# Performance work log

Hardware: AMD Instinct MI355X
Metric: run time of the kernel (lower is better)

## Reference

```python
import jax, jax.numpy as jnp
import numpy as np

H = 256          # hidden_channels
NP, NJ, NC = 8192, 8192, 4096  # person / job_posting / company node counts
EA, EW, EP = 262144, 131072, 131072  # edge counts per relation


def _gcn(x_src, W, b, edge_index, num_src, num_dst):
    """Bipartite GCNConv: h = x_src @ W; out[dst] = sum_e norm_e * h[src_e] + b,
    norm = deg_out(src)^-1/2 * deg_in(dst)^-1/2 (symmetric GCN normalization)."""
    h = x_src @ W                                # [num_src, H]
    row, col = edge_index[0], edge_index[1]
    ones = jnp.ones(row.shape[0], dtype=h.dtype)
    deg_src = jax.ops.segment_sum(ones, row, num_segments=num_src)
    deg_dst = jax.ops.segment_sum(ones, col, num_segments=num_dst)
    dis_src = jnp.where(deg_src > 0, jax.lax.rsqrt(jnp.maximum(deg_src, 1e-12)), 0.0)
    dis_dst = jnp.where(deg_dst > 0, jax.lax.rsqrt(jnp.maximum(deg_dst, 1e-12)), 0.0)
    norm = dis_src[row] * dis_dst[col]           # [E]
    out = jax.ops.segment_sum(h[row] * norm[:, None], col, num_segments=num_dst)
    return out + b


def setup_inputs() -> dict:
    key = jax.random.key(0)
    ks = jax.random.split(key, 12)
    s = 1.0 / np.sqrt(H)
    return {
        "x_person":  jax.random.normal(ks[0], (NP, H), jnp.float32),
        "x_job":     jax.random.normal(ks[1], (NJ, H), jnp.float32),
        "x_company": jax.random.normal(ks[2], (NC, H), jnp.float32),
        "ei_applied": jax.random.randint(ks[3], (2, EA), 0, 8192, jnp.int64 if jax.config.read('jax_enable_x64') else jnp.int32),
        "ei_worked":  jax.random.randint(ks[4], (2, EW), 0, 4096, jnp.int64 if jax.config.read('jax_enable_x64') else jnp.int32),
        "ei_posted":  jax.random.randint(ks[5], (2, EP), 0, 4096, jnp.int64 if jax.config.read('jax_enable_x64') else jnp.int32),
        "W_aj": jax.random.normal(ks[6], (H, H), jnp.float32) * s,
        "b_aj": jnp.zeros((H,), jnp.float32),
        "W_wa": jax.random.normal(ks[7], (H, H), jnp.float32) * s,
        "b_wa": jnp.zeros((H,), jnp.float32),
        "W_pb": jax.random.normal(ks[8], (H, H), jnp.float32) * s,
        "b_pb": jnp.zeros((H,), jnp.float32),
    }


def reference(x_person, x_job, x_company, ei_applied, ei_worked, ei_posted,
              W_aj, b_aj, W_wa, b_wa, W_pb, b_pb):
    Np, Nj, Nc = x_person.shape[0], x_job.shape[0], x_company.shape[0]
    # HeteroConv with aggr='sum': each dst type sums messages over its edge types
    job_emb = _gcn(x_person, W_aj, b_aj, ei_applied, Np, Nj)
    comp_emb = (_gcn(x_person, W_wa, b_wa, ei_worked, Np, Nc)
                + _gcn(x_job, W_pb, b_pb, ei_posted, Nj, Nc))  # computed but unused downstream
    del comp_emb
    person_emb = x_person  # 'person' is never a dst type; features pass through
    scores = jax.nn.sigmoid(person_emb @ job_emb.T)  # [Np, Nj]
    return scores
```

## Files before the change

### kernel.cpp

```cpp
#include <hip/hip_runtime.h>
#include <hip/hip_bf16.h>

#define HCH 256
#define NPN 8192
#define NJN 8192
#define EAE 262144

typedef _Float16 f16x8 __attribute__((ext_vector_type(8)));
typedef _Float16 f16x4 __attribute__((ext_vector_type(4)));
typedef _Float16 f16x2 __attribute__((ext_vector_type(2)));
typedef float f32x4 __attribute__((ext_vector_type(4)));

#define WS_DEG_SRC   0
#define WS_DEG_DST   32768
#define WS_CUR       65536
#define WS_OFFS      98304
#define WS_DIS_SRC   131328
#define WS_DIS_DST   164096
#define WS_CSR       196864
#define WS_XH        1245440
#define WS_ZH        5439744
#define WS_GH        9634048
#define WS_WHT       13828352

__global__ void k_zero(int* p) {
    int i = blockIdx.x * 256 + threadIdx.x;
    p[i] = 0;
}

__global__ void k_count(const int* __restrict__ row, const int* __restrict__ col,
                        int* deg_src, int* deg_dst) {
    int e = blockIdx.x * 256 + threadIdx.x;
    if (e < EAE) {
        atomicAdd(&deg_src[row[e]], 1);
        atomicAdd(&deg_dst[col[e]], 1);
    }
}

__global__ void k_prep(const int* __restrict__ deg_src, const int* __restrict__ deg_dst,
                       int* __restrict__ offs, float* __restrict__ dis_src,
                       float* __restrict__ dis_dst, const float* __restrict__ W,
                       _Float16* __restrict__ WhT, const float* __restrict__ x,
                       _Float16* __restrict__ Xh) {
    int bid = blockIdx.x;
    int t = threadIdx.x;
    if (bid == 0) {
        __shared__ int part[256];
        int base = t * 32;
        int local[32];
        int s = 0;
#pragma unroll
        for (int i = 0; i < 32; i++) { local[i] = s; s += deg_dst[base + i]; }
        part[t] = s;
        __syncthreads();
        for (int d = 1; d < 256; d <<= 1) {
            int self = part[t];
            int add = (t >= d) ? part[t - d] : 0;
            __syncthreads();
            part[t] = self + add;
            __syncthreads();
        }
        int chunk_excl = (t > 0) ? part[t - 1] : 0;
#pragma unroll
        for (int i = 0; i < 32; i++) offs[base + i] = chunk_excl + local[i];
        if (t == 255) offs[NJN] = part[255];
    } else if (bid < 65) {
        int i = (bid - 1) * 256 + t;
        if (i < NPN) {
            int d = deg_src[i];
            dis_src[i] = d > 0 ? rsqrtf((float)d) : 0.f;
        } else {
            int j = i - NPN;
            int d = deg_dst[j];
            dis_dst[j] = d > 0 ? rsqrtf((float)d) : 0.f;
        }
    } else if (bid < 321) {
        int idx = (bid - 65) * 256 + t;
        int n = idx >> 8, k = idx & 255;
        WhT[idx] = (_Float16)W[k * HCH + n];
    } else {
        int i = ((bid - 321) * 256 + t) * 4;
        float4 v = *(const float4*)(x + i);
        f16x4 h;
        h[0] = (_Float16)v.x; h[1] = (_Float16)v.y;
        h[2] = (_Float16)v.z; h[3] = (_Float16)v.w;
        *(f16x4*)(Xh + i) = h;
    }
}

__global__ void k_bucket(const int* __restrict__ row, const int* __restrict__ col,
                         const int* __restrict__ offs, int* cur, int* csr) {
    int e = blockIdx.x * 256 + threadIdx.x;
    if (e < EAE) {
        int c = col[e];
        int p = atomicAdd(&cur[c], 1);
        csr[offs[c] + p] = row[e];
    }
}

__global__ void k_agg(const _Float16* __restrict__ Xh, const int* __restrict__ csr,
                      const int* __restrict__ offs, const float* __restrict__ dis_src,
                      const float* __restrict__ dis_dst, _Float16* __restrict__ Zh) {
    int j = blockIdx.x;
    int c = threadIdx.x;
    int e0 = offs[j], e1 = offs[j + 1];
    float a0 = 0.f, a1 = 0.f;
    int e = e0;
    for (; e + 1 < e1; e += 2) {
        int s0 = csr[e], s1 = csr[e + 1];
        float w0 = dis_src[s0], w1 = dis_src[s1];
        f16x2 v0 = *(const f16x2*)(Xh + (size_t)s0 * HCH + 2 * c);
        f16x2 v1 = *(const f16x2*)(Xh + (size_t)s1 * HCH + 2 * c);
        a0 += w0 * (float)v0[0] + w1 * (float)v1[0];
        a1 += w0 * (float)v0[1] + w1 * (float)v1[1];
    }
    if (e < e1) {
        int s0 = csr[e];
        float w0 = dis_src[s0];
        f16x2 v0 = *(const f16x2*)(Xh + (size_t)s0 * HCH + 2 * c);
        a0 += w0 * (float)v0[0];
        a1 += w0 * (float)v0[1];
    }
    float dd = dis_dst[j];
    f16x2 out;
    out[0] = (_Float16)(a0 * dd);
    out[1] = (_Float16)(a1 * dd);
    *(f16x2*)(Zh + (size_t)j * HCH + 2 * c) = out;
}

template <bool SIGMOID>
__global__ __launch_bounds__(256, 2)
void k_gemm(const _Float16* __restrict__ A, const _Float16* __restrict__ Bt,
            const float* __restrict__ bias, void* __restrict__ Cout, int Ncols) {
    __shared__ _Float16 smA[128 * 64];
    __shared__ _Float16 smB[128 * 64];
    int tid = threadIdx.x;
    int wid = tid >> 6, lane = tid & 63;

    int bx = blockIdx.x, by = blockIdx.y;
    if (SIGMOID) {
        int nbx = gridDim.x;
        int lin = by * nbx + bx;
        int chunk = (nbx * gridDim.y) >> 3;
        int swz = (lin & 7) * chunk + (lin >> 3);
        bx = swz % nbx;
        by = swz / nbx;
    }
    int brow = by * 128;
    int bcol = bx * 128;
    int wrow = (wid >> 1) * 64;
    int wcol = (wid & 1) * 64;

    f32x4 acc[4][4] = {};

    int lr = lane & 15;
    int kq = lane >> 4;

    for (int k0 = 0; k0 < HCH; k0 += 64) {
        __syncthreads();
#pragma unroll
        for (int i = 0; i < 4; i++) {
            int cch = tid + i * 256;
            int r = cch >> 3, cc = cch & 7;
            int byteoff = (r * 128 + cc * 16) ^ ((r & 7) << 4);
            uint4 va = *(const uint4*)(A + (size_t)(brow + r) * HCH + k0 + cc * 8);
            *(uint4*)((char*)smA + byteoff) = va;
            uint4 vb = *(const uint4*)(Bt + (size_t)(bcol + r) * HCH + k0 + cc * 8);
            *(uint4*)((char*)smB + byteoff) = vb;
        }
        __syncthreads();
#pragma unroll
        for (int kk = 0; kk < 64; kk += 32) {
            f16x8 af[4], bfr[4];
            int kbyte = (kk + kq * 8) * 2;
#pragma unroll
            for (int m = 0; m < 4; m++) {
                int r = wrow + m * 16 + lr;
                int byteoff = (r * 128 + kbyte) ^ ((r & 7) << 4);
                af[m] = *(const f16x8*)((const char*)smA + byteoff);
            }
#pragma unroll
            for (int n = 0; n < 4; n++) {
                int r = wcol + n * 16 + lr;
                int byteoff = (r * 128 + kbyte) ^ ((r & 7) << 4);
                bfr[n] = *(const f16x8*)((const char*)smB + byteoff);
            }
#pragma unroll
            for (int m = 0; m < 4; m++)
#pragma unroll
                for (int n = 0; n < 4; n++)
                    acc[m][n] = __builtin_amdgcn_mfma_f32_16x16x32_f16(
                        af[m], bfr[n], acc[m][n], 0, 0, 0);
        }
    }

    int rq = lane >> 4;
#pragma unroll
    for (int m = 0; m < 4; m++) {
#pragma unroll
        for (int n = 0; n < 4; n++) {
#pragma unroll
            for (int j = 0; j < 4; j++) {
                int gr = brow + wrow + m * 16 + rq * 4 + j;
                int gc = bcol + wcol + n * 16 + lr;
                float v = acc[m][n][j];
                if (SIGMOID) {
                    ((float*)Cout)[(size_t)gr * Ncols + gc] = 1.f / (1.f + __expf(-v));
                } else {
                    v += bias[gc];
                    ((_Float16*)Cout)[(size_t)gr * Ncols + gc] = (_Float16)v;
                }
            }
        }
    }
}

extern "C" void kernel_launch(void* const* d_in, const int* in_sizes, int n_in,
                              void* d_out, int out_size, void* d_ws, size_t ws_size,
                              hipStream_t stream) {
    const float* x_person = (const float*)d_in[0];
    const int*   ei_app   = (const int*)d_in[3];
    const float* W_aj     = (const float*)d_in[6];
    const float* b_aj     = (const float*)d_in[7];

    const int* erow = ei_app;
    const int* ecol = ei_app + EAE;

    char* w = (char*)d_ws;
    int*   deg_src = (int*)(w + WS_DEG_SRC);
    int*   deg_dst = (int*)(w + WS_DEG_DST);
    int*   cur     = (int*)(w + WS_CUR);
    int*   offs    = (int*)(w + WS_OFFS);
    float* dis_src = (float*)(w + WS_DIS_SRC);
    float* dis_dst = (float*)(w + WS_DIS_DST);
    int*   csr     = (int*)(w + WS_CSR);
    _Float16* Xh   = (_Float16*)(w + WS_XH);
    _Float16* Zh   = (_Float16*)(w + WS_ZH);
    _Float16* Gh   = (_Float16*)(w + WS_GH);
    _Float16* WhT  = (_Float16*)(w + WS_WHT);

    k_zero<<<96, 256, 0, stream>>>((int*)w);
    k_count<<<EAE / 256, 256, 0, stream>>>(erow, ecol, deg_src, deg_dst);
    k_prep<<<2369, 256, 0, stream>>>(deg_src, deg_dst, offs, dis_src, dis_dst,
                                     W_aj, WhT, x_person, Xh);
    k_bucket<<<EAE / 256, 256, 0, stream>>>(erow, ecol, offs, cur, csr);
    k_agg<<<NJN, 128, 0, stream>>>(Xh, csr, offs, dis_src, dis_dst, Zh);
    {
        dim3 grid(HCH / 128, NJN / 128);
        k_gemm<false><<<grid, 256, 0, stream>>>(Zh, WhT, b_aj, (void*)Gh, HCH);
    }
    {
        dim3 grid(NJN / 128, NPN / 128);
        k_gemm<true><<<grid, 256, 0, stream>>>(Xh, Gh, nullptr, d_out, NJN);
    }
}
```

Baseline: 154.8 us.

## Load GEMM tiles directly global-to-LDS and use fast reciprocal sigmoid

The GEMM's tile loads now use global_load_lds, which copies global memory straight into LDS with no register round trip. Because that instruction writes LDS linearly per wave, the XOR swizzle is dropped and fragments are read from an unswizzled layout. The change also skips the first redundant barrier, raises the occupancy hint to 3 blocks per CU, and replaces the sigmoid division with a hardware reciprocal. The risks are LDS bank conflicts on the unswizzled reads, register pressure under the tighter launch bound, and a slight loss of precision in the sigmoid.

```diff
diff --git a/kernel.cpp b/kernel.cpp
--- a/kernel.cpp
+++ b/kernel.cpp
@@ -10,6 +10,9 @@
 typedef _Float16 f16x4 __attribute__((ext_vector_type(4)));
 typedef _Float16 f16x2 __attribute__((ext_vector_type(2)));
 typedef float f32x4 __attribute__((ext_vector_type(4)));
+
+typedef __attribute__((address_space(1))) void glb_void;
+typedef __attribute__((address_space(3))) void lds_void;
 
 #define WS_DEG_SRC   0
 #define WS_DEG_DST   32768
@@ -129,7 +132,7 @@
 }
 
 template <bool SIGMOID>
-__global__ __launch_bounds__(256, 2)
+__global__ __launch_bounds__(256, 3)
 void k_gemm(const _Float16* __restrict__ A, const _Float16* __restrict__ Bt,
             const float* __restrict__ bias, void* __restrict__ Cout, int Ncols) {
     __shared__ _Float16 smA[128 * 64];
@@ -157,16 +160,20 @@
     int kq = lane >> 4;
 
     for (int k0 = 0; k0 < HCH; k0 += 64) {
-        __syncthreads();
+        if (k0) __syncthreads();
 #pragma unroll
         for (int i = 0; i < 4; i++) {
-            int cch = tid + i * 256;
-            int r = cch >> 3, cc = cch & 7;
-            int byteoff = (r * 128 + cc * 16) ^ ((r & 7) << 4);
-            uint4 va = *(const uint4*)(A + (size_t)(brow + r) * HCH + k0 + cc * 8);
-            *(uint4*)((char*)smA + byteoff) = va;
-            uint4 vb = *(const uint4*)(Bt + (size_t)(bcol + r) * HCH + k0 + cc * 8);
-            *(uint4*)((char*)smB + byteoff) = vb;
+            int wc0 = i * 256 + wid * 64;
+            int c = wc0 + lane;
+            int r = c >> 3, cc = c & 7;
+            const char* ga = (const char*)A +
+                (size_t)(brow + r) * (HCH * 2) + (size_t)(k0 + cc * 8) * 2;
+            const char* gb = (const char*)Bt +
+                (size_t)(bcol + r) * (HCH * 2) + (size_t)(k0 + cc * 8) * 2;
+            __builtin_amdgcn_global_load_lds(
+                (glb_void*)ga, (lds_void*)((char*)smA + wc0 * 16), 16, 0, 0);
+            __builtin_amdgcn_global_load_lds(
+                (glb_void*)gb, (lds_void*)((char*)smB + wc0 * 16), 16, 0, 0);
         }
         __syncthreads();
 #pragma unroll
@@ -176,14 +183,12 @@
 #pragma unroll
             for (int m = 0; m < 4; m++) {
                 int r = wrow + m * 16 + lr;
-                int byteoff = (r * 128 + kbyte) ^ ((r & 7) << 4);
-                af[m] = *(const f16x8*)((const char*)smA + byteoff);
+                af[m] = *(const f16x8*)((const char*)smA + r * 128 + kbyte);
             }
 #pragma unroll
             for (int n = 0; n < 4; n++) {
                 int r = wcol + n * 16 + lr;
-                int byteoff = (r * 128 + kbyte) ^ ((r & 7) << 4);
-                bfr[n] = *(const f16x8*)((const char*)smB + byteoff);
+                bfr[n] = *(const f16x8*)((const char*)smB + r * 128 + kbyte);
             }
 #pragma unroll
             for (int m = 0; m < 4; m++)
@@ -205,7 +210,9 @@
                 int gc = bcol + wcol + n * 16 + lr;
                 float v = acc[m][n][j];
                 if (SIGMOID) {
-                    ((float*)Cout)[(size_t)gr * Ncols + gc] = 1.f / (1.f + __expf(-v));
+                    float e = __expf(-v);
+                    ((float*)Cout)[(size_t)gr * Ncols + gc] =
+                        __builtin_amdgcn_rcpf(1.f + e);
                 } else {
                     v += bias[gc];
                     ((_Float16*)Cout)[(size_t)gr * Ncols + gc] = (_Float16)v;
```

Result: no change. 151.8 us (-1.9%).
